# Optimization experiments

Measured on AMD Instinct MI355X. Metric: run time of the kernel, lower is better.

## Reference

```python
import jax, jax.numpy as jnp
import numpy as np

B, T, IN, HID, HYP = 32, 1024, 512, 512, 256


def setup_inputs() -> dict:
    key = jax.random.key(0)
    ks = jax.random.split(key, 12)
    s = lambda *sh: 1.0 / np.sqrt(sh[-1])
    return {
        "x": jax.random.normal(ks[0], (B, T, IN), jnp.float32),
        "hidden": jax.random.normal(ks[1], (B, HID), jnp.float32),
        "W_start": jax.random.uniform(ks[2], (HYP, IN), jnp.float32, -s(HYP, IN), s(HYP, IN)),
        "b_start": jax.random.uniform(ks[3], (HYP,), jnp.float32, -s(HYP, IN), s(HYP, IN)),
        "W_mid": jax.random.uniform(ks[4], (HYP, HYP), jnp.float32, -s(HYP, HYP), s(HYP, HYP)),
        "b_mid": jax.random.uniform(ks[5], (HYP,), jnp.float32, -s(HYP, HYP), s(HYP, HYP)),
        "W_end": jax.random.uniform(ks[6], (HID, HYP), jnp.float32, -s(HID, HYP), s(HID, HYP)),
        "b_end": jax.random.uniform(ks[7], (HID,), jnp.float32, -s(HID, HYP), s(HID, HYP)),
        "W2": jax.random.uniform(ks[8], (HID, IN), jnp.float32, -s(HID, IN), s(HID, IN)),
        "b2": jax.random.uniform(ks[9], (HID,), jnp.float32, -s(HID, IN), s(HID, IN)),
    }


def _roll_sum_relu(b, hidden):
    # b: [B, T, H], hidden: [B, H]
    # recurrence: h_t = relu(roll(h_{t-1}, 1, axis=-1) + b_t)
    bt = jnp.swapaxes(b, 0, 1)  # [T, B, H]

    def step(h, b_t):
        h_new = jax.nn.relu(jnp.roll(h, 1, axis=-1) + b_t)
        return h_new, h_new

    _, outs = jax.lax.scan(step, hidden, bt)
    return jnp.swapaxes(outs, 0, 1)  # [B, T, H]


def reference(x, hidden, W_start, b_start, W_mid, b_mid, W_end, b_end, W2, b2):
    h = jax.nn.relu(jnp.einsum('bti,hi->bth', x, W_start) + b_start)
    h = jax.nn.relu(jnp.einsum('bth,gh->btg', h, W_mid) + b_mid)
    fc_end = jnp.einsum('btg,og->bto', h, W_end) + b_end
    sig = jax.nn.sigmoid(jnp.einsum('bti,oi->bto', x, W2) + b2)
    b = fc_end * sig  # [B, T, HID]
    outputs = _roll_sum_relu(b, hidden)
    return outputs, outputs[:, -1, :]
```

## Files before the change

### kernel.cpp

```cpp
#include <hip/hip_runtime.h>
#include <math.h>

#define B_   32
#define T_   1024
#define IN_  512
#define HID_ 512
#define HYP_ 256
#define M_   (B_ * T_)
#define R_   128
#define NSEG 8
#define SEGL 128
#define NCH  (B_ * HID_)

#define H1S  0
#define H2S  65536
#define STG  131072
#define LDS_BYTES 163840

typedef _Float16 half8_t __attribute__((ext_vector_type(8)));
typedef float    f32x4   __attribute__((ext_vector_type(4)));

typedef __attribute__((address_space(1))) const void* gptr_as1;
typedef __attribute__((address_space(3))) void*       lptr_as3;

__device__ __forceinline__ void gload_lds16(const void* g, void* l) {
    __builtin_amdgcn_global_load_lds((gptr_as1)g, (lptr_as3)l, 16, 0, 0);
}

#define VMCNT6() asm volatile("s_waitcnt vmcnt(6)" ::: "memory")
#define VMCNT4() asm volatile("s_waitcnt vmcnt(4)" ::: "memory")
#define VMCNT0() asm volatile("s_waitcnt vmcnt(0)" ::: "memory")
#define SBAR()   __builtin_amdgcn_s_barrier()
#define SCHED0() __builtin_amdgcn_sched_barrier(0)

__global__ __launch_bounds__(256) void cvt_all(
    const float* __restrict__ x,  _Float16* __restrict__ xh,
    const float* __restrict__ Ws, _Float16* __restrict__ wsh,
    const float* __restrict__ Wm, _Float16* __restrict__ wmh,
    const float* __restrict__ We, _Float16* __restrict__ weh,
    const float* __restrict__ W2, _Float16* __restrict__ w2h)
{
    const int blk = blockIdx.x;
    const float* src; _Float16* dst; int base;
    if      (blk < 8192) { src = x;  dst = xh;  base = blk; }
    else if (blk < 8256) { src = Ws; dst = wsh; base = blk - 8192; }
    else if (blk < 8288) { src = Wm; dst = wmh; base = blk - 8256; }
    else if (blk < 8352) { src = We; dst = weh; base = blk - 8288; }
    else                 { src = W2; dst = w2h; base = blk - 8352; }
    const int i = base * 2048 + threadIdx.x * 8;
    f32x4 v0 = *(const f32x4*)(src + i);
    f32x4 v1 = *(const f32x4*)(src + i + 4);
    half8_t h;
    h[0] = (_Float16)v0[0]; h[1] = (_Float16)v0[1];
    h[2] = (_Float16)v0[2]; h[3] = (_Float16)v0[3];
    h[4] = (_Float16)v1[0]; h[5] = (_Float16)v1[1];
    h[6] = (_Float16)v1[2]; h[7] = (_Float16)v1[3];
    *(half8_t*)(dst + i) = h;
}

__device__ __forceinline__ void stage512(const _Float16* src, int K,
                                         char* ldsbase, int tid)
{
#pragma unroll
    for (int q = 0; q < 2; ++q) {
        const int s = q * 512 + tid;
        const int g = s >> 6, c2 = (s >> 4) & 3, r = (s & 15) ^ c2;
        const char* gp = (const char*)src + (size_t)(g * 16 + r) * (K * 2) + c2 * 16;
        char* lp = ldsbase + (q * 512 + (tid & ~63)) * 16;
        gload_lds16(gp, lp);
    }
}

__device__ __forceinline__ void stageA(const _Float16* src, int K,
                                       char* ldsbase, int tid)
{
    const int s = tid;
    const int g = s >> 6, c2 = (s >> 4) & 3, r = (s & 15) ^ c2;
    const char* gp = (const char*)src + (size_t)(g * 16 + r) * (K * 2) + c2 * 16;
    char* lp = ldsbase + (tid & ~63) * 16;
    gload_lds16(gp, lp);
}

__device__ __forceinline__ void stageA64(const _Float16* src, int K,
                                         char* ldsbase, int tid)
{
    stageA(src,      K, ldsbase,        tid);
    stageA(src + 32, K, ldsbase + 8192, tid);
}

__device__ __forceinline__ void stageW64(const _Float16* src, int K,
                                         char* ldsbase, int tid)
{
    stage512(src,      K, ldsbase,         tid);
    stage512(src + 32, K, ldsbase + 16384, tid);
}

__device__ __forceinline__ void do_step16(const char* ab, const char* bb,
                                          int wm, int wn, int lsw,
                                          f32x4 acc[4][4])
{
    half8_t af[4], wf[4];
#pragma unroll
    for (int i = 0; i < 4; ++i)
        af[i] = *(const half8_t*)(ab + (wm * 4 + i) * 1024 + lsw);
#pragma unroll
    for (int j = 0; j < 4; ++j)
        wf[j] = *(const half8_t*)(bb + (wn * 4 + j) * 1024 + lsw);
#pragma unroll
    for (int i = 0; i < 4; ++i)
#pragma unroll
        for (int j = 0; j < 4; ++j)
            acc[i][j] = __builtin_amdgcn_mfma_f32_16x16x32_f16(af[i], wf[j], acc[i][j], 0, 0, 0);
}

__device__ __forceinline__ void do_step32(const char* ab, const char* bb,
                                          int wm, int wn, int lsw,
                                          f32x4 acc[4][4])
{
    do_step16(ab,        bb,         wm, wn, lsw, acc);
    do_step16(ab + 8192, bb + 16384, wm, wn, lsw, acc);
}

__device__ __forceinline__ void epi_relu_lds(char* dst, const f32x4 acc[4][4],
                                             const float* __restrict__ bias,
                                             int wm, int wn, int lq, int lr)
{
#pragma unroll
    for (int j = 0; j < 4; ++j) {
        const int col = wn * 64 + j * 16 + lr;
        const float bv = bias[col];
        const int cc2 = (col & 31) >> 3;
        const int cpart = (col >> 5) * 8192 + cc2 * 256 + (col & 7) * 2;
#pragma unroll
        for (int i = 0; i < 4; ++i) {
#pragma unroll
            for (int rg = 0; rg < 4; ++rg) {
                const int row = wm * 64 + i * 16 + lq * 4 + rg;
                const float v = fmaxf(acc[i][j][rg] + bv, 0.f);
                *(_Float16*)(dst + cpart + (row >> 4) * 1024 +
                             (((row & 15) ^ cc2)) * 16) = (_Float16)v;
            }
        }
    }
}

__global__ __launch_bounds__(512, 2) void fused_mlp(
    const _Float16* __restrict__ xh,
    const _Float16* __restrict__ wsh, const float* __restrict__ bs,
    const _Float16* __restrict__ wmh, const float* __restrict__ bm,
    const _Float16* __restrict__ weh, const float* __restrict__ be,
    const _Float16* __restrict__ w2h, const float* __restrict__ b2,
    _Float16* __restrict__ bh)
{
    __shared__ __align__(16) char lds[LDS_BYTES];

    const int tid  = threadIdx.x;
    const int m0   = blockIdx.x * R_;
    const int lane = tid & 63;
    const int wave = tid >> 6;
    const int wm = wave >> 2;
    const int wn = wave & 3;
    const int lq = lane >> 4, lr = lane & 15;
    const int lsw = (lane ^ ((lane >> 4) & 3)) * 16;

    const _Float16* xrow = xh + (size_t)m0 * IN_;
    const f32x4 zero = {0.f, 0.f, 0.f, 0.f};

    {
        f32x4 acc[4][4];
#pragma unroll
        for (int i = 0; i < 4; ++i)
#pragma unroll
            for (int j = 0; j < 4; ++j) acc[i][j] = zero;

        stageA64(xrow, IN_, lds + H2S, tid);
        stageW64(wsh, IN_, lds + STG, tid);
        for (int s = 0; s < 7; ++s) {
            const int e = s + 1;
            stageA64(xrow + e * 64, IN_, lds + H2S + (e & 1) * 16384, tid);
            stageW64(wsh + e * 64, IN_, (e & 1) ? lds + H2S + 32768 : lds + STG, tid);
            VMCNT6(); SCHED0(); SBAR(); SCHED0();
            const char* ab = lds + H2S + (s & 1) * 16384;
            const char* bb = (s & 1) ? lds + H2S + 32768 : lds + STG;
            __builtin_amdgcn_s_setprio(1);
            do_step32(ab, bb, wm, wn, lsw, acc);
            __builtin_amdgcn_s_setprio(0);
            SCHED0(); SBAR(); SCHED0();
        }
        stageW64(wmh, HYP_, lds + STG, tid);
        VMCNT4(); SCHED0(); SBAR(); SCHED0();
        __builtin_amdgcn_s_setprio(1);
        do_step32(lds + H2S + 16384, lds + H2S + 32768, wm, wn, lsw, acc);
        __builtin_amdgcn_s_setprio(0);
        __syncthreads();
        epi_relu_lds(lds + H1S, acc, bs, wm, wn, lq, lr);
        __syncthreads();
    }

    {
        f32x4 acc[4][4];
#pragma unroll
        for (int i = 0; i < 4; ++i)
#pragma unroll
            for (int j = 0; j < 4; ++j) acc[i][j] = zero;

        for (int s = 0; s < 3; ++s) {
            const int e = s + 1;
            stageW64(wmh + e * 64, HYP_, (e & 1) ? lds + H2S : lds + STG, tid);
            VMCNT4(); SCHED0(); SBAR(); SCHED0();
            const char* ab = lds + H1S + s * 16384;
            const char* bb = (s & 1) ? lds + H2S : lds + STG;
            __builtin_amdgcn_s_setprio(1);
            do_step32(ab, bb, wm, wn, lsw, acc);
            __builtin_amdgcn_s_setprio(0);
            SCHED0(); SBAR(); SCHED0();
        }
        stageW64(weh, HYP_, lds + STG, tid);
        VMCNT4(); SCHED0(); SBAR(); SCHED0();
        __builtin_amdgcn_s_setprio(1);
        do_step32(lds + H1S + 49152, lds + H2S, wm, wn, lsw, acc);
        __builtin_amdgcn_s_setprio(0);
        __syncthreads();
        epi_relu_lds(lds + H2S, acc, bm, wm, wn, lq, lr);
        __syncthreads();
    }

#pragma unroll 1
    for (int half = 0; half < 2; ++half) {
        const int c0 = half * 256;
        const _Float16* wehh = weh + (size_t)c0 * HYP_;
        const _Float16* w2hh = w2h + (size_t)c0 * IN_;
        f32x4 accf[4][4], accs[4][4];
#pragma unroll
        for (int i = 0; i < 4; ++i)
#pragma unroll
            for (int j = 0; j < 4; ++j) { accf[i][j] = zero; accs[i][j] = zero; }

        for (int s = 0; s < 3; ++s) {
            const int e = s + 1;
            stageW64(wehh + e * 64, HYP_, (e & 1) ? lds + H1S : lds + STG, tid);
            VMCNT4(); SCHED0(); SBAR(); SCHED0();
            const char* ab = lds + H2S + s * 16384;
            const char* bb = (s & 1) ? lds + H1S : lds + STG;
            __builtin_amdgcn_s_setprio(1);
            do_step32(ab, bb, wm, wn, lsw, accf);
            __builtin_amdgcn_s_setprio(0);
            SCHED0(); SBAR(); SCHED0();
        }
        stageA64(xrow, IN_, lds + H1S + 32768, tid);
        stageW64(w2hh, IN_, lds + STG, tid);
        VMCNT6(); SCHED0(); SBAR(); SCHED0();
        __builtin_amdgcn_s_setprio(1);
        do_step32(lds + H2S + 49152, lds + H1S, wm, wn, lsw, accf);
        __builtin_amdgcn_s_setprio(0);
        SCHED0(); SBAR(); SCHED0();

        for (int s = 0; s < 7; ++s) {
            const int e = s + 1;
            stageA64(xrow + e * 64, IN_, lds + H1S + 32768 + (e & 1) * 16384, tid);
            stageW64(w2hh + e * 64, IN_, (e & 1) ? lds + H1S : lds + STG, tid);
            VMCNT6(); SCHED0(); SBAR(); SCHED0();
            const char* ab = lds + H1S + 32768 + (s & 1) * 16384;
            const char* bb = (s & 1) ? lds + H1S : lds + STG;
            __builtin_amdgcn_s_setprio(1);
            do_step32(ab, bb, wm, wn, lsw, accs);
            __builtin_amdgcn_s_setprio(0);
            SCHED0(); SBAR(); SCHED0();
        }
        if (half == 0) {
            stageW64(weh + (size_t)256 * HYP_, HYP_, lds + STG, tid);
            VMCNT4();
        } else {
            VMCNT0();
        }
        SCHED0(); SBAR(); SCHED0();
        __builtin_amdgcn_s_setprio(1);
        do_step32(lds + H1S + 49152, lds + H1S, wm, wn, lsw, accs);
        __builtin_amdgcn_s_setprio(0);
        __syncthreads();

#pragma unroll
        for (int j = 0; j < 4; ++j) {
            const int gcol = c0 + wn * 64 + j * 16 + lr;
            const float bev = be[gcol];
            const float b2v = b2[gcol];
#pragma unroll
            for (int i = 0; i < 4; ++i) {
#pragma unroll
                for (int rg = 0; rg < 4; ++rg) {
                    const int row = m0 + wm * 64 + i * 16 + lq * 4 + rg;
                    const float fc = accf[i][j][rg] + bev;
                    float sg = accs[i][j][rg] + b2v;
                    sg = 1.f / (1.f + __expf(-sg));
                    bh[(size_t)row * HID_ + gcol] = (_Float16)(fc * sg);
                }
            }
        }
        __syncthreads();
    }
}

__global__ __launch_bounds__(256) void seg_reduce(const _Float16* __restrict__ bh,
                                                  float* __restrict__ Sarr,
                                                  float* __restrict__ Darr)
{
    const int G = blockIdx.x * 256 + threadIdx.x;
    const int r = G & 511;
    const int seg = (G >> 9) & 7;
    const int b = G >> 12;
    const int chain = b * 512 + r;
    const _Float16* bb = bh + (size_t)b * (T_ * HID_);
    const int t0 = seg * SEGL;

    float S = 0.f, D = -__builtin_inff();
#pragma unroll 8
    for (int u = 0; u < SEGL; ++u) {
        const int t = t0 + u;
        const float v = (float)bb[t * 512 + ((r + t) & 511)];
        S += v;
        D = fmaxf(D + v, 0.f);
    }
    Sarr[seg * NCH + chain] = S;
    Darr[seg * NCH + chain] = D;
}

__global__ __launch_bounds__(64) void carry_scan(const float* __restrict__ hidden,
                                                 const float* __restrict__ Sarr,
                                                 const float* __restrict__ Darr,
                                                 float* __restrict__ carry,
                                                 float* __restrict__ hlast)
{
    const int chain = blockIdx.x * 64 + threadIdx.x;
    const int b = chain >> 9, r = chain & 511;
    float c = hidden[b * 512 + ((r + 511) & 511)];
#pragma unroll
    for (int j = 0; j < NSEG; ++j) {
        carry[j * NCH + chain] = c;
        c = fmaxf(c + Sarr[j * NCH + chain], Darr[j * NCH + chain]);
    }
    hlast[b * 512 + ((r + 1023) & 511)] = c;
}

__global__ __launch_bounds__(256) void seg_apply(const _Float16* __restrict__ bh,
                                                 const float* __restrict__ carry,
                                                 float* __restrict__ out)
{
    const int G = blockIdx.x * 256 + threadIdx.x;
    const int r = G & 511;
    const int seg = (G >> 9) & 7;
    const int b = G >> 12;
    const int chain = b * 512 + r;
    const _Float16* bb = bh + (size_t)b * (T_ * HID_);
    float* ob = out + (size_t)b * (T_ * HID_);
    const int t0 = seg * SEGL;

    float c = carry[seg * NCH + chain];
#pragma unroll 8
    for (int u = 0; u < SEGL; ++u) {
        const int t = t0 + u;
        const int idx = t * 512 + ((r + t) & 511);
        c = fmaxf(c + (float)bb[idx], 0.f);
        ob[idx] = c;
    }
}

extern "C" void kernel_launch(void* const* d_in, const int* in_sizes, int n_in,
                              void* d_out, int out_size, void* d_ws, size_t ws_size,
                              hipStream_t stream)
{
    const float* x      = (const float*)d_in[0];
    const float* hidden = (const float*)d_in[1];
    const float* Ws     = (const float*)d_in[2];
    const float* bs     = (const float*)d_in[3];
    const float* Wm     = (const float*)d_in[4];
    const float* bm     = (const float*)d_in[5];
    const float* We     = (const float*)d_in[6];
    const float* be     = (const float*)d_in[7];
    const float* W2     = (const float*)d_in[8];
    const float* b2     = (const float*)d_in[9];

    float* outputs = (float*)d_out;
    float* hlast   = outputs + (size_t)M_ * HID_;

    _Float16* xh = (_Float16*)d_out;

    _Float16* bh   = (_Float16*)d_ws;
    _Float16* wsh  = bh + (size_t)M_ * HID_;
    _Float16* wmh  = wsh + HYP_ * IN_;
    _Float16* weh  = wmh + HYP_ * HYP_;
    _Float16* w2h  = weh + HID_ * HYP_;
    float*    Sarr = (float*)(w2h + HID_ * IN_);
    float*    Darr = Sarr + NSEG * NCH;
    float*    carr = Darr + NSEG * NCH;

    cvt_all<<<dim3(8480), 256, 0, stream>>>(x, xh, Ws, wsh, Wm, wmh, We, weh, W2, w2h);
    fused_mlp<<<dim3(M_ / R_), 512, 0, stream>>>(
        xh, wsh, bs, wmh, bm, weh, be, w2h, b2, bh);
    seg_reduce<<<dim3((NCH * NSEG) / 256), 256, 0, stream>>>(bh, Sarr, Darr);
    carry_scan<<<dim3(NCH / 64), 64, 0, stream>>>(hidden, Sarr, Darr, carr, hlast);
    seg_apply<<<dim3((NCH * NSEG) / 256), 256, 0, stream>>>(bh, carr, outputs);
}
```

Baseline: 117.7 us.

## Fuse x fp32-to-fp16 conversion into MLP kernel A-tile staging

Drops the separate pass that converted all of x to fp16 in global memory. The fused MLP kernel now loads fp32 x rows into registers, converts them, and writes fp16 tiles into LDS. These register loads are issued ahead of the weight prefetch, and the wait counts and barriers are adjusted to match. This removes a full write and reread of a 32 MB fp16 copy of x, but the fp32 reads are twice as wide, and the extra LDS stores plus lgkmcnt waits sit inside the pipelined loop.

```diff
diff --git a/kernel.cpp b/kernel.cpp
--- a/kernel.cpp
+++ b/kernel.cpp
@@ -27,14 +27,14 @@
     __builtin_amdgcn_global_load_lds((gptr_as1)g, (lptr_as3)l, 16, 0, 0);
 }
 
-#define VMCNT6() asm volatile("s_waitcnt vmcnt(6)" ::: "memory")
+#define VMCNT8() asm volatile("s_waitcnt vmcnt(8)" ::: "memory")
 #define VMCNT4() asm volatile("s_waitcnt vmcnt(4)" ::: "memory")
 #define VMCNT0() asm volatile("s_waitcnt vmcnt(0)" ::: "memory")
+#define LGKM0()  asm volatile("s_waitcnt lgkmcnt(0)" ::: "memory")
 #define SBAR()   __builtin_amdgcn_s_barrier()
 #define SCHED0() __builtin_amdgcn_sched_barrier(0)
 
-__global__ __launch_bounds__(256) void cvt_all(
-    const float* __restrict__ x,  _Float16* __restrict__ xh,
+__global__ __launch_bounds__(256) void cvt_w(
     const float* __restrict__ Ws, _Float16* __restrict__ wsh,
     const float* __restrict__ Wm, _Float16* __restrict__ wmh,
     const float* __restrict__ We, _Float16* __restrict__ weh,
@@ -42,11 +42,10 @@
 {
     const int blk = blockIdx.x;
     const float* src; _Float16* dst; int base;
-    if      (blk < 8192) { src = x;  dst = xh;  base = blk; }
-    else if (blk < 8256) { src = Ws; dst = wsh; base = blk - 8192; }
-    else if (blk < 8288) { src = Wm; dst = wmh; base = blk - 8256; }
-    else if (blk < 8352) { src = We; dst = weh; base = blk - 8288; }
-    else                 { src = W2; dst = w2h; base = blk - 8352; }
+    if      (blk < 64)  { src = Ws; dst = wsh; base = blk; }
+    else if (blk < 96)  { src = Wm; dst = wmh; base = blk - 64; }
+    else if (blk < 160) { src = We; dst = weh; base = blk - 96; }
+    else                { src = W2; dst = w2h; base = blk - 160; }
     const int i = base * 2048 + threadIdx.x * 8;
     f32x4 v0 = *(const f32x4*)(src + i);
     f32x4 v1 = *(const f32x4*)(src + i + 4);
@@ -71,28 +70,31 @@
     }
 }
 
-__device__ __forceinline__ void stageA(const _Float16* src, int K,
-                                       char* ldsbase, int tid)
-{
-    const int s = tid;
-    const int g = s >> 6, c2 = (s >> 4) & 3, r = (s & 15) ^ c2;
-    const char* gp = (const char*)src + (size_t)(g * 16 + r) * (K * 2) + c2 * 16;
-    char* lp = ldsbase + (tid & ~63) * 16;
-    gload_lds16(gp, lp);
-}
-
-__device__ __forceinline__ void stageA64(const _Float16* src, int K,
-                                         char* ldsbase, int tid)
-{
-    stageA(src,      K, ldsbase,        tid);
-    stageA(src + 32, K, ldsbase + 8192, tid);
-}
-
 __device__ __forceinline__ void stageW64(const _Float16* src, int K,
                                          char* ldsbase, int tid)
 {
     stage512(src,      K, ldsbase,         tid);
     stage512(src + 32, K, ldsbase + 16384, tid);
+}
+
+__device__ __forceinline__ void ld_x32(const float* __restrict__ x, int m0,
+                                       int ks, int tid, f32x4& a, f32x4& b)
+{
+    const int g = tid >> 6, c2 = (tid >> 4) & 3, r = (tid & 15) ^ c2;
+    const float* p = x + (size_t)(m0 + g * 16 + r) * IN_ + ks + c2 * 8;
+    a = *(const f32x4*)p;
+    b = *(const f32x4*)(p + 4);
+}
+
+__device__ __forceinline__ void wr_x32(const f32x4& a, const f32x4& b,
+                                       char* ldsbase, int tid)
+{
+    half8_t h;
+    h[0] = (_Float16)a[0]; h[1] = (_Float16)a[1];
+    h[2] = (_Float16)a[2]; h[3] = (_Float16)a[3];
+    h[4] = (_Float16)b[0]; h[5] = (_Float16)b[1];
+    h[6] = (_Float16)b[2]; h[7] = (_Float16)b[3];
+    *(half8_t*)(ldsbase + tid * 16) = h;
 }
 
 __device__ __forceinline__ void do_step16(const char* ab, const char* bb,
@@ -145,7 +147,7 @@
 }
 
 __global__ __launch_bounds__(512, 2) void fused_mlp(
-    const _Float16* __restrict__ xh,
+    const float* __restrict__ x,
     const _Float16* __restrict__ wsh, const float* __restrict__ bs,
     const _Float16* __restrict__ wmh, const float* __restrict__ bm,
     const _Float16* __restrict__ weh, const float* __restrict__ be,
@@ -163,7 +165,6 @@
     const int lq = lane >> 4, lr = lane & 15;
     const int lsw = (lane ^ ((lane >> 4) & 3)) * 16;
 
-    const _Float16* xrow = xh + (size_t)m0 * IN_;
     const f32x4 zero = {0.f, 0.f, 0.f, 0.f};
 
     {
@@ -173,22 +174,35 @@
 #pragma unroll
             for (int j = 0; j < 4; ++j) acc[i][j] = zero;
 
-        stageA64(xrow, IN_, lds + H2S, tid);
-        stageW64(wsh, IN_, lds + STG, tid);
+        {
+            f32x4 pa0, pa1, pa2, pa3;
+            ld_x32(x, m0, 0, tid, pa0, pa1);
+            ld_x32(x, m0, 32, tid, pa2, pa3);
+            stageW64(wsh, IN_, lds + STG, tid);
+            wr_x32(pa0, pa1, lds + H2S, tid);
+            wr_x32(pa2, pa3, lds + H2S + 8192, tid);
+            __syncthreads();
+        }
         for (int s = 0; s < 7; ++s) {
             const int e = s + 1;
-            stageA64(xrow + e * 64, IN_, lds + H2S + (e & 1) * 16384, tid);
+            f32x4 pa0, pa1, pa2, pa3;
+            ld_x32(x, m0, e * 64, tid, pa0, pa1);
+            ld_x32(x, m0, e * 64 + 32, tid, pa2, pa3);
+            SCHED0();
             stageW64(wsh + e * 64, IN_, (e & 1) ? lds + H2S + 32768 : lds + STG, tid);
-            VMCNT6(); SCHED0(); SBAR(); SCHED0();
+            SCHED0(); VMCNT8(); SCHED0(); SBAR(); SCHED0();
+            char* xb = lds + H2S + (e & 1) * 16384;
+            wr_x32(pa0, pa1, xb, tid);
+            wr_x32(pa2, pa3, xb + 8192, tid);
             const char* ab = lds + H2S + (s & 1) * 16384;
             const char* bb = (s & 1) ? lds + H2S + 32768 : lds + STG;
             __builtin_amdgcn_s_setprio(1);
             do_step32(ab, bb, wm, wn, lsw, acc);
             __builtin_amdgcn_s_setprio(0);
-            SCHED0(); SBAR(); SCHED0();
+            LGKM0(); SCHED0(); SBAR(); SCHED0();
         }
         stageW64(wmh, HYP_, lds + STG, tid);
-        VMCNT4(); SCHED0(); SBAR(); SCHED0();
+        SCHED0(); VMCNT4(); SCHED0(); SBAR(); SCHED0();
         __builtin_amdgcn_s_setprio(1);
         do_step32(lds + H2S + 16384, lds + H2S + 32768, wm, wn, lsw, acc);
         __builtin_amdgcn_s_setprio(0);
@@ -207,7 +221,7 @@
         for (int s = 0; s < 3; ++s) {
             const int e = s + 1;
             stageW64(wmh + e * 64, HYP_, (e & 1) ? lds + H2S : lds + STG, tid);
-            VMCNT4(); SCHED0(); SBAR(); SCHED0();
+            SCHED0(); VMCNT4(); SCHED0(); SBAR(); SCHED0();
             const char* ab = lds + H1S + s * 16384;
             const char* bb = (s & 1) ? lds + H2S : lds + STG;
             __builtin_amdgcn_s_setprio(1);
@@ -216,7 +230,7 @@
             SCHED0(); SBAR(); SCHED0();
         }
         stageW64(weh, HYP_, lds + STG, tid);
-        VMCNT4(); SCHED0(); SBAR(); SCHED0();
+        SCHED0(); VMCNT4(); SCHED0(); SBAR(); SCHED0();
         __builtin_amdgcn_s_setprio(1);
         do_step32(lds + H1S + 49152, lds + H2S, wm, wn, lsw, acc);
         __builtin_amdgcn_s_setprio(0);
@@ -239,7 +253,7 @@
         for (int s = 0; s < 3; ++s) {
             const int e = s + 1;
             stageW64(wehh + e * 64, HYP_, (e & 1) ? lds + H1S : lds + STG, tid);
-            VMCNT4(); SCHED0(); SBAR(); SCHED0();
+            SCHED0(); VMCNT4(); SCHED0(); SBAR(); SCHED0();
             const char* ab = lds + H2S + s * 16384;
             const char* bb = (s & 1) ? lds + H1S : lds + STG;
             __builtin_amdgcn_s_setprio(1);
@@ -247,29 +261,41 @@
             __builtin_amdgcn_s_setprio(0);
             SCHED0(); SBAR(); SCHED0();
         }
-        stageA64(xrow, IN_, lds + H1S + 32768, tid);
-        stageW64(w2hh, IN_, lds + STG, tid);
-        VMCNT6(); SCHED0(); SBAR(); SCHED0();
-        __builtin_amdgcn_s_setprio(1);
-        do_step32(lds + H2S + 49152, lds + H1S, wm, wn, lsw, accf);
-        __builtin_amdgcn_s_setprio(0);
-        SCHED0(); SBAR(); SCHED0();
-
+        {
+            f32x4 pa0, pa1, pa2, pa3;
+            ld_x32(x, m0, 0, tid, pa0, pa1);
+            ld_x32(x, m0, 32, tid, pa2, pa3);
+            SCHED0();
+            stageW64(w2hh, IN_, lds + STG, tid);
+            SCHED0(); VMCNT8(); SCHED0(); SBAR(); SCHED0();
+            wr_x32(pa0, pa1, lds + H1S + 32768, tid);
+            wr_x32(pa2, pa3, lds + H1S + 32768 + 8192, tid);
+            __builtin_amdgcn_s_setprio(1);
+            do_step32(lds + H2S + 49152, lds + H1S, wm, wn, lsw, accf);
+            __builtin_amdgcn_s_setprio(0);
+            LGKM0(); SCHED0(); SBAR(); SCHED0();
+        }
         for (int s = 0; s < 7; ++s) {
             const int e = s + 1;
-            stageA64(xrow + e * 64, IN_, lds + H1S + 32768 + (e & 1) * 16384, tid);
+            f32x4 pa0, pa1, pa2, pa3;
+            ld_x32(x, m0, e * 64, tid, pa0, pa1);
+            ld_x32(x, m0, e * 64 + 32, tid, pa2, pa3);
+            SCHED0();
             stageW64(w2hh + e * 64, IN_, (e & 1) ? lds + H1S : lds + STG, tid);
-            VMCNT6(); SCHED0(); SBAR(); SCHED0();
+            SCHED0(); VMCNT8(); SCHED0(); SBAR(); SCHED0();
+            char* xb = lds + H1S + 32768 + (e & 1) * 16384;
+            wr_x32(pa0, pa1, xb, tid);
+            wr_x32(pa2, pa3, xb + 8192, tid);
             const char* ab = lds + H1S + 32768 + (s & 1) * 16384;
             const char* bb = (s & 1) ? lds + H1S : lds + STG;
             __builtin_amdgcn_s_setprio(1);
             do_step32(ab, bb, wm, wn, lsw, accs);
             __builtin_amdgcn_s_setprio(0);
-            SCHED0(); SBAR(); SCHED0();
+            LGKM0(); SCHED0(); SBAR(); SCHED0();
         }
         if (half == 0) {
             stageW64(weh + (size_t)256 * HYP_, HYP_, lds + STG, tid);
-            VMCNT4();
+            SCHED0(); VMCNT4();
         } else {
             VMCNT0();
         }
@@ -382,8 +408,6 @@
     float* outputs = (float*)d_out;
     float* hlast   = outputs + (size_t)M_ * HID_;
 
-    _Float16* xh = (_Float16*)d_out;
-
     _Float16* bh   = (_Float16*)d_ws;
     _Float16* wsh  = bh + (size_t)M_ * HID_;
     _Float16* wmh  = wsh + HYP_ * IN_;
@@ -393,9 +417,9 @@
     float*    Darr = Sarr + NSEG * NCH;
     float*    carr = Darr + NSEG * NCH;
 
-    cvt_all<<<dim3(8480), 256, 0, stream>>>(x, xh, Ws, wsh, Wm, wmh, We, weh, W2, w2h);
+    cvt_w<<<dim3(288), 256, 0, stream>>>(Ws, wsh, Wm, wmh, We, weh, W2, w2h);
     fused_mlp<<<dim3(M_ / R_), 512, 0, stream>>>(
-        xh, wsh, bs, wmh, bm, weh, be, w2h, b2, bh);
+        x, wsh, bs, wmh, bm, weh, be, w2h, b2, bh);
     seg_reduce<<<dim3((NCH * NSEG) / 256), 256, 0, stream>>>(bh, Sarr, Darr);
     carry_scan<<<dim3(NCH / 64), 64, 0, stream>>>(hidden, Sarr, Darr, carr, hlast);
     seg_apply<<<dim3((NCH * NSEG) / 256), 256, 0, stream>>>(bh, carr, outputs);
```

Result: slower. 126.9 us (+7.7%).
